# Kernel tuning notes

Measured on AMD Instinct MI355X. Metric: run time of the kernel, lower is better.

## Reference

```python
import jax, jax.numpy as jnp
from jax import lax
import numpy as np

B, D, P = 4096, 256, 512  # batch, encoded_space_dim (=d_prototypes), n_prototypes
BN_EPS = 1e-5  # torch BatchNorm eval with running_mean=0, running_var=1


def _conv(x, w, stride, pad):
    # x: NCHW, w: OIHW
    return lax.conv_general_dilated(x, w, (stride, stride), [(pad, pad), (pad, pad)],
                                    dimension_numbers=('NCHW', 'OIHW', 'NCHW'))


def _conv_t(x, w, stride, pad, out_pad):
    # torch ConvTranspose2d; w in torch layout [Cin, Cout, kh, kw]
    k = w.shape[2]
    wf = jnp.flip(w, (2, 3)).transpose(1, 0, 2, 3)  # -> OIHW, flipped
    lo = k - 1 - pad
    hi = k - 1 - pad + out_pad
    return lax.conv_general_dilated(x, wf, (1, 1), [(lo, hi), (lo, hi)],
                                    lhs_dilation=(stride, stride),
                                    dimension_numbers=('NCHW', 'OIHW', 'NCHW'))


def _bn(x, g, b):
    # eval-mode BatchNorm2d with running_mean=0, running_var=1
    s = g / jnp.sqrt(1.0 + BN_EPS)
    return x * s[None, :, None, None] + b[None, :, None, None]


def _bias(x, b):
    return x + b[None, :, None, None]


def setup_inputs() -> dict:
    key = jax.random.key(0)
    ks = jax.random.split(key, 32)
    n = jax.random.normal
    inp = {
        'x': jax.random.uniform(ks[0], (B, 1, 28, 28), jnp.float32),
        # encoder
        'w1': n(ks[1], (8, 1, 3, 3), jnp.float32) * 0.1, 'b1': jnp.zeros((8,), jnp.float32),
        'w2': n(ks[2], (16, 8, 3, 3), jnp.float32) * 0.1, 'b2': jnp.zeros((16,), jnp.float32),
        'g2': jnp.ones((16,), jnp.float32), 'bt2': jnp.zeros((16,), jnp.float32),
        'w3': n(ks[3], (D, 16, 3, 3), jnp.float32) * 0.1, 'b3': jnp.zeros((D,), jnp.float32),
        # prototypes (torch.rand init)
        'protolayer': jax.random.uniform(ks[4], (P, D, 1, 1), jnp.float32),
        # up layer (ConvTranspose2d(D, D, 5), torch layout [Cin,Cout,kh,kw])
        'wup': n(ks[5], (D, D, 5, 5), jnp.float32) * 0.02, 'bup': jnp.zeros((D,), jnp.float32),
        'gup': jnp.ones((D,), jnp.float32), 'btup': jnp.zeros((D,), jnp.float32),
        # decoder
        'wd1': n(ks[6], (D, 16, 3, 3), jnp.float32) * 0.05, 'bd1': jnp.zeros((16,), jnp.float32),
        'gd1': jnp.ones((16,), jnp.float32), 'btd1': jnp.zeros((16,), jnp.float32),
        'wd2': n(ks[7], (16, 8, 3, 3), jnp.float32) * 0.1, 'bd2': jnp.zeros((8,), jnp.float32),
        'gd2': jnp.ones((8,), jnp.float32), 'btd2': jnp.zeros((8,), jnp.float32),
        'wd3': n(ks[8], (8, 1, 3, 3), jnp.float32) * 0.1, 'bd3': jnp.zeros((1,), jnp.float32),
    }
    return inp


def reference(x, w1, b1, w2, b2, g2, bt2, w3, b3, protolayer,
              wup, bup, gup, btup,
              wd1, bd1, gd1, btd1, wd2, bd2, gd2, btd2, wd3, bd3):
    # ---- encoder: 28 -> 14 -> 7 -> 5 ----
    h = jax.nn.relu(_bias(_conv(x, w1, 2, 1), b1))
    h = jax.nn.relu(_bn(_bias(_conv(h, w2, 2, 1), b2), g2, bt2))
    h = jax.nn.relu(_bias(_conv(h, w3, 1, 0), b3))  # [B, D, 5, 5]

    # ---- l2 'convolution' with 1x1 prototypes ----
    p = protolayer[:, :, 0, 0]                                  # [P, D]
    x2_patch_sum = jnp.sum(h * h, axis=1)                       # ones-conv, 1x1 kernel -> channel sum [B,5,5]
    xp = jnp.einsum('bdhw,pd->bphw', h, p)                      # [B, P, 5, 5]
    p2 = jnp.sum(p * p, axis=1)                                 # [P]
    distances = jax.nn.relu(x2_patch_sum[:, None] - 2.0 * xp + p2[None, :, None, None])

    # min-pool over full spatial extent
    min_distances = jnp.min(distances, axis=(2, 3))             # [B, P]
    prototype_activations = -min_distances                      # 'linear' distance_2_similarity
    w = jax.nn.softmax(prototype_activations, axis=1)
    z = jnp.einsum('bp,pdkl->bdkl', w, protolayer)              # [B, D, 1, 1]

    # ---- up layer: 1 -> 5 ----
    z = jax.nn.relu(_bn(_bias(_conv_t(z, wup, 1, 0, 0), bup), gup, btup))

    # ---- decoder: 5 -> 7 -> 14 -> 28 ----
    h = jax.nn.relu(_bn(_bias(_conv_t(z, wd1, 1, 0, 0), bd1), gd1, btd1))
    h = jax.nn.relu(_bn(_bias(_conv_t(h, wd2, 2, 1, 1), bd2), gd2, btd2))
    out = jax.nn.sigmoid(_bias(_conv_t(h, wd3, 2, 1, 1), bd3))  # [B, 1, 28, 28]
    return out, min_distances
```

## Files before the change

kernel.cpp:

```cpp
#include <hip/hip_runtime.h>
#include <hip/hip_bf16.h>
#include <math.h>

#define NB 4096
#define DC 256
#define PC 512

typedef unsigned short ushort_t;
typedef __attribute__((ext_vector_type(4))) unsigned short us4;
typedef __attribute__((ext_vector_type(8))) unsigned short us8;
typedef __attribute__((ext_vector_type(8))) short s8v;
typedef __attribute__((ext_vector_type(4))) float f32x4;

__device__ __forceinline__ float bf16_to_f(ushort_t u) {
    union { unsigned int i; float f; } c;
    c.i = ((unsigned int)u) << 16;
    return c.f;
}
__device__ __forceinline__ ushort_t f2bf(float f) {
    union { float f; unsigned int u; } c; c.f = f;
    unsigned int r = c.u + 0x7fffu + ((c.u >> 16) & 1u);
    return (ushort_t)(r >> 16);
}

__global__ __launch_bounds__(256) void k_pre(
    const float* __restrict__ proto, float* __restrict__ p2,
    ushort_t* __restrict__ pfragHi, ushort_t* __restrict__ pfragLo,
    const float* __restrict__ w3, ushort_t* __restrict__ w3fH, ushort_t* __restrict__ w3fL,
    const float* __restrict__ w2, ushort_t* __restrict__ w2fH, ushort_t* __restrict__ w2fL,
    const float* __restrict__ wd1, ushort_t* __restrict__ wd1frag,
    const float* __restrict__ wup, ushort_t* __restrict__ wupfH, ushort_t* __restrict__ wupfL)
{
    int b = blockIdx.x, tid = threadIdx.x;
    __shared__ float red[256];
    if (b < 512) {
        int p = b, d = tid;
        float v = proto[p * DC + d];
        red[d] = v * v;
        __syncthreads();
        for (int s = 128; s > 0; s >>= 1) {
            if (d < s) red[d] += red[d + s];
            __syncthreads();
        }
        if (d == 0) p2[p] = red[0];
    } else if (b < 1024) {
        int idx = (b - 512) * 256 + tid;
        int j = idx & 7, l = (idx >> 3) & 63;
        int k0 = (idx >> 9) & 7, nt = idx >> 12;
        int n = nt * 16 + (l & 15);
        int k = k0 * 32 + (l >> 4) * 8 + j;
        float v = proto[n * DC + k];
        ushort_t hi = f2bf(v);
        pfragHi[idx] = hi;
        pfragLo[idx] = f2bf(v - bf16_to_f(hi));
    } else if (b < 1184) {
        int idx = (b - 1024) * 256 + tid;
        int j = idx & 7, l = (idx >> 3) & 63;
        int q = idx >> 9;
        int k0 = q % 5, nt = q / 5;
        int d = nt * 16 + (l & 15);
        int k = k0 * 32 + (l >> 4) * 8 + j;
        float v = (k < 144) ? w3[d * 144 + k] : 0.f;
        ushort_t hi = f2bf(v);
        w3fH[idx] = hi;
        w3fL[idx] = f2bf(v - bf16_to_f(hi));
    } else if (b < 1190) {
        int idx = (b - 1184) * 256 + tid;
        int j = idx & 7, l = (idx >> 3) & 63;
        int k0 = idx >> 9;
        int ch = l & 15;
        int k = k0 * 32 + (l >> 4) * 8 + j;
        float v = (k < 72) ? w2[ch * 72 + k] : 0.f;
        ushort_t hi = f2bf(v);
        w2fH[idx] = hi;
        w2fL[idx] = f2bf(v - bf16_to_f(hi));
    } else if (b < 1334) {
        int idx = (b - 1190) * 256 + tid;
        int j = idx & 7, l = (idx >> 3) & 63;
        int k0 = (idx >> 9) & 7, nt = idx >> 12;
        int n = nt * 16 + (l & 15);
        int k = k0 * 32 + (l >> 4) * 8 + j;
        wd1frag[idx] = f2bf(wd1[k * 144 + n]);
    } else {
        int idx = (b - 1334) * 256 + tid;
        int j = idx & 7, l = (idx >> 3) & 63;
        int k0 = (idx >> 9) & 7, nt = idx >> 12;
        int np = nt * 16 + (l & 15);
        int d = k0 * 32 + (l >> 4) * 8 + j;
        int pos = np >> 8, ch = np & 255;
        float v = wup[d * 6400 + ch * 25 + pos];
        ushort_t hi = f2bf(v);
        wupfH[idx] = hi;
        wupfL[idx] = f2bf(v - bf16_to_f(hi));
    }
}

__global__ __launch_bounds__(256) void k_pw2(
    const ushort_t* __restrict__ pfragHi, const ushort_t* __restrict__ pfragLo,
    const ushort_t* __restrict__ wupfH, const ushort_t* __restrict__ wupfL,
    ushort_t* __restrict__ PWfrag)
{
    int t = threadIdx.x;
    int w = t >> 6, l = t & 63, lr = l & 15, lg = l >> 4;
    int my = blockIdx.y;
    int ntb = blockIdx.x * 16 + w * 4;
    const s8v* AH = (const s8v*)pfragHi;
    const s8v* AL = (const s8v*)pfragLo;
    const s8v* BH = (const s8v*)wupfH;
    const s8v* BL = (const s8v*)wupfL;
    f32x4 acc[4];
#pragma unroll
    for (int q = 0; q < 4; q++) acc[q] = (f32x4){0.f, 0.f, 0.f, 0.f};
#pragma unroll
    for (int k0 = 0; k0 < 8; k0++) {
        s8v ah = AH[(my * 8 + k0) * 64 + l];
        s8v al = AL[(my * 8 + k0) * 64 + l];
#pragma unroll
        for (int q = 0; q < 4; q++) {
            s8v bh = BH[(size_t)((ntb + q) * 8 + k0) * 64 + l];
            s8v bl = BL[(size_t)((ntb + q) * 8 + k0) * 64 + l];
            acc[q] = __builtin_amdgcn_mfma_f32_16x16x32_bf16(ah, bh, acc[q], 0, 0, 0);
            acc[q] = __builtin_amdgcn_mfma_f32_16x16x32_bf16(al, bh, acc[q], 0, 0, 0);
            acc[q] = __builtin_amdgcn_mfma_f32_16x16x32_bf16(ah, bl, acc[q], 0, 0, 0);
        }
    }
#pragma unroll
    for (int q = 0; q < 4; q++) {
        int nt = ntb + q;
#pragma unroll
        for (int r = 0; r < 4; r++) {
            int p = my * 16 + lg * 4 + r;
            int k0p = p >> 5;
            int ll = ((p >> 3) & 3) * 16 + lr;
            int jj = p & 7;
            PWfrag[(((size_t)(nt * 16 + k0p) * 64) + ll) * 8 + jj] = f2bf(acc[q][r]);
        }
    }
}

__global__ __launch_bounds__(512) void k_enc1(
    const float* __restrict__ x,
    const float* __restrict__ w1, const float* __restrict__ b1,
    const ushort_t* __restrict__ w2fH, const ushort_t* __restrict__ w2fL,
    const float* __restrict__ b2,
    const float* __restrict__ g2, const float* __restrict__ bt2,
    const ushort_t* __restrict__ w3fH, const ushort_t* __restrict__ w3fL,
    const float* __restrict__ b3,
    ushort_t* __restrict__ h3g)
{
    int b0 = blockIdx.x * 2;
    int t = threadIdx.x;
    int w = t >> 6, l = t & 63, lr = l & 15, lg = l >> 4;
    int tim = t >> 8, tt = t & 255;

    __shared__ __align__(16) unsigned char buf[51712];
    unsigned char* bufI = buf + tim * 25856;
    float* xb = (float*)bufI;
    float* h1 = (float*)(bufI + 3136);
    ushort_t* im2Hi = (ushort_t*)(bufI + 9408);
    float* h2 = (float*)(bufI + 22720);
    ushort_t* imHi = (ushort_t*)bufI;

    const float bnr = rsqrtf(1.0f + 1e-5f);

    const float* xg = x + (size_t)(b0 + tim) * 784;
    for (int i = tt; i < 784; i += 256) xb[i] = xg[i];
    for (int i = tt; i < 832; i += 256)
        ((float4*)(bufI + 9408))[i] = (float4){0.f, 0.f, 0.f, 0.f};
    __syncthreads();

    for (int o = tt; o < 1568; o += 256) {
        int c = o / 196, r = o % 196, y = r / 14, xc = r % 14;
        float acc = b1[c];
        for (int sy = 0; sy < 3; sy++) {
            int iy = 2 * y - 1 + sy;
            if ((unsigned)iy >= 28u) continue;
            for (int sx = 0; sx < 3; sx++) {
                int ix = 2 * xc - 1 + sx;
                if ((unsigned)ix >= 28u) continue;
                acc += w1[c * 9 + sy * 3 + sx] * xb[iy * 28 + ix];
            }
        }
        float v = fmaxf(acc, 0.f);
        ushort_t hi = f2bf(v);
        int kb = c * 9;
        int yA, syA, xA, sxA, yB = 0, xB = 0;
        bool hasYB, hasXB;
        if (y & 1) { yA = y >> 1; syA = 2; yB = yA + 1; hasYB = (yB < 7); }
        else       { yA = y >> 1; syA = 1; hasYB = false; }
        if (xc & 1) { xA = xc >> 1; sxA = 2; xB = xA + 1; hasXB = (xB < 7); }
        else        { xA = xc >> 1; sxA = 1; hasXB = false; }
        im2Hi[(yA * 7 + xA) * 104 + kb + syA * 3 + sxA] = hi;
        if (hasXB) im2Hi[(yA * 7 + xB) * 104 + kb + syA * 3] = hi;
        if (hasYB) {
            im2Hi[(yB * 7 + xA) * 104 + kb + sxA] = hi;
            if (hasXB) im2Hi[(yB * 7 + xB) * 104 + kb] = hi;
        }
    }
    __syncthreads();

    {
        int w4 = w & 3;
        f32x4 cc = {0, 0, 0, 0};
        const s8v* WH = (const s8v*)w2fH;
        const s8v* WL = (const s8v*)w2fL;
#pragma unroll
        for (int k0 = 0; k0 < 3; k0++) {
            s8v a0 = *(const s8v*)&im2Hi[(w4 * 16 + lr) * 104 + k0 * 32 + lg * 8];
            s8v bh = WH[k0 * 64 + l];
            s8v bl = WL[k0 * 64 + l];
            cc = __builtin_amdgcn_mfma_f32_16x16x32_bf16(a0, bh, cc, 0, 0, 0);
            cc = __builtin_amdgcn_mfma_f32_16x16x32_bf16(a0, bl, cc, 0, 0, 0);
        }
        int ch = lr;
        float s = g2[ch] * bnr, bb = b2[ch], bt = bt2[ch];
#pragma unroll
        for (int r = 0; r < 4; r++) {
            int pos = w4 * 16 + lg * 4 + r;
            if (pos < 49)
                h2[ch * 49 + pos] = fmaxf((cc[r] + bb) * s + bt, 0.f);
        }
    }
    __syncthreads();

    if (tt < 16) imHi[3600 + tt] = 0;
    for (int o = tt; o < 784; o += 256) {
        float v = h2[o];
        int ci = o / 49, rr = o % 49, iy = rr / 7, ixp = rr % 7;
        ushort_t hi = f2bf(v);
        int kb = ci * 9;
#pragma unroll
        for (int sy = 0; sy < 3; sy++) {
            int py = iy - sy;
            if ((unsigned)py < 5u) {
#pragma unroll
                for (int sx = 0; sx < 3; sx++) {
                    int px = ixp - sx;
                    if ((unsigned)px < 5u)
                        imHi[(py * 5 + px) * 144 + kb + sy * 3 + sx] = hi;
                }
            }
        }
    }
    __syncthreads();

    {
        const ushort_t* imHi0 = (const ushort_t*)buf;
        const ushort_t* imHi1 = (const ushort_t*)(buf + 25856);
        int nt0 = 2 * w;
        f32x4 c[2][2][2];
#pragma unroll
        for (int im = 0; im < 2; im++)
#pragma unroll
            for (int q = 0; q < 2; q++)
#pragma unroll
                for (int mt = 0; mt < 2; mt++) c[im][q][mt] = (f32x4){0.f, 0.f, 0.f, 0.f};
        const s8v* WH = (const s8v*)w3fH;
        const s8v* WL = (const s8v*)w3fL;
#pragma unroll
        for (int k0 = 0; k0 < 5; k0++) {
            s8v a00 = *(const s8v*)&imHi0[lr * 144 + k0 * 32 + lg * 8];
            s8v a01 = *(const s8v*)&imHi0[(16 + lr) * 144 + k0 * 32 + lg * 8];
            s8v a10 = *(const s8v*)&imHi1[lr * 144 + k0 * 32 + lg * 8];
            s8v a11 = *(const s8v*)&imHi1[(16 + lr) * 144 + k0 * 32 + lg * 8];
            s8v bh0 = WH[(nt0 * 5 + k0) * 64 + l];
            s8v bl0 = WL[(nt0 * 5 + k0) * 64 + l];
            s8v bh1 = WH[((nt0 + 1) * 5 + k0) * 64 + l];
            s8v bl1 = WL[((nt0 + 1) * 5 + k0) * 64 + l];
            c[0][0][0] = __builtin_amdgcn_mfma_f32_16x16x32_bf16(a00, bh0, c[0][0][0], 0, 0, 0);
            c[0][0][1] = __builtin_amdgcn_mfma_f32_16x16x32_bf16(a01, bh0, c[0][0][1], 0, 0, 0);
            c[0][0][0] = __builtin_amdgcn_mfma_f32_16x16x32_bf16(a00, bl0, c[0][0][0], 0, 0, 0);
            c[0][0][1] = __builtin_amdgcn_mfma_f32_16x16x32_bf16(a01, bl0, c[0][0][1], 0, 0, 0);
            c[0][1][0] = __builtin_amdgcn_mfma_f32_16x16x32_bf16(a00, bh1, c[0][1][0], 0, 0, 0);
            c[0][1][1] = __builtin_amdgcn_mfma_f32_16x16x32_bf16(a01, bh1, c[0][1][1], 0, 0, 0);
            c[0][1][0] = __builtin_amdgcn_mfma_f32_16x16x32_bf16(a00, bl1, c[0][1][0], 0, 0, 0);
            c[0][1][1] = __builtin_amdgcn_mfma_f32_16x16x32_bf16(a01, bl1, c[0][1][1], 0, 0, 0);
            c[1][0][0] = __builtin_amdgcn_mfma_f32_16x16x32_bf16(a10, bh0, c[1][0][0], 0, 0, 0);
            c[1][0][1] = __builtin_amdgcn_mfma_f32_16x16x32_bf16(a11, bh0, c[1][0][1], 0, 0, 0);
            c[1][0][0] = __builtin_amdgcn_mfma_f32_16x16x32_bf16(a10, bl0, c[1][0][0], 0, 0, 0);
            c[1][0][1] = __builtin_amdgcn_mfma_f32_16x16x32_bf16(a11, bl0, c[1][0][1], 0, 0, 0);
            c[1][1][0] = __builtin_amdgcn_mfma_f32_16x16x32_bf16(a10, bh1, c[1][1][0], 0, 0, 0);
            c[1][1][1] = __builtin_amdgcn_mfma_f32_16x16x32_bf16(a11, bh1, c[1][1][1], 0, 0, 0);
            c[1][1][0] = __builtin_amdgcn_mfma_f32_16x16x32_bf16(a10, bl1, c[1][1][0], 0, 0, 0);
            c[1][1][1] = __builtin_amdgcn_mfma_f32_16x16x32_bf16(a11, bl1, c[1][1][1], 0, 0, 0);
        }
#pragma unroll
        for (int im = 0; im < 2; im++) {
            ushort_t* hg = h3g + (size_t)(b0 + im) * 6400;
#pragma unroll
            for (int q = 0; q < 2; q++) {
                int d = (nt0 + q) * 16 + lr;
                float bb = b3[d];
#pragma unroll
                for (int mt = 0; mt < 2; mt++) {
                    f32x4 cv = c[im][q][mt];
#pragma unroll
                    for (int r = 0; r < 4; r++) {
                        int pos = mt * 16 + lg * 4 + r;
                        if (pos < 25) {
                            float h = fmaxf(cv[r] + bb, 0.f);
                            hg[pos * 256 + d] = f2bf(h);
                        }
                    }
                }
            }
        }
    }
}

__global__ __launch_bounds__(1024) void k_enc2(
    const ushort_t* __restrict__ h3g,
    const ushort_t* __restrict__ pfragHi,
    const float* __restrict__ p2,
    float* __restrict__ md_out,
    ushort_t* __restrict__ Wsm)
{
    int t = threadIdx.x;
    int b0 = blockIdx.x * 2;
    int w = t >> 6, l = t & 63, lr = l & 15, lg = l >> 4;

    __shared__ __align__(16) ushort_t h3s[2][32][264];
    __shared__ float mds[2][512];
    __shared__ float x2sh[2][32];
    __shared__ float x2part[2][25][8];
    __shared__ float wred[2][16];

    for (int i = t; i < 2048; i += 1024) {
        int im = i >> 10, pos = (i >> 5) & 31, c8 = i & 31;
        us8 v = {0, 0, 0, 0, 0, 0, 0, 0};
        if (pos < 25)
            v = *(const us8*)&h3g[(size_t)(b0 + im) * 6400 + pos * 256 + c8 * 8];
        *(us8*)&h3s[im][pos][c8 * 8] = v;
    }
    __syncthreads();

    if (t < 400) {
        int im = t / 200, rest = t % 200;
        int pos = rest >> 3, ch = rest & 7;
        const ushort_t* hp = &h3s[im][pos][ch * 32];
        float s = 0.f;
#pragma unroll
        for (int i = 0; i < 32; i++) {
            float f = bf16_to_f(hp[i]);
            s = fmaf(f, f, s);
        }
        x2part[im][pos][ch] = s;
    }
    __syncthreads();
    if (t < 64) {
        int im = t >> 5, pos = t & 31;
        float s = 1e30f;
        if (pos < 25) {
            s = 0.f;
#pragma unroll
            for (int c = 0; c < 8; c++) s += x2part[im][pos][c];
        }
        x2sh[im][pos] = s;
    }
    __syncthreads();

    {
        f32x4 acc[2][2][2];
#pragma unroll
        for (int i = 0; i < 2; i++)
#pragma unroll
            for (int jm = 0; jm < 2; jm++)
#pragma unroll
                for (int mt = 0; mt < 2; mt++) acc[i][jm][mt] = (f32x4){0.f, 0.f, 0.f, 0.f};
        const s8v* BH = (const s8v*)pfragHi;
        s8v bhc[2], bhn[2];
#pragma unroll
        for (int ntq = 0; ntq < 2; ntq++) {
            int nt = w * 2 + ntq;
            bhc[ntq] = BH[(nt * 8 + 0) * 64 + l];
        }
        for (int k0 = 0; k0 < 8; k0++) {
            if (k0 < 7) {
#pragma unroll
                for (int ntq = 0; ntq < 2; ntq++) {
                    int nt = w * 2 + ntq;
                    bhn[ntq] = BH[(nt * 8 + k0 + 1) * 64 + l];
                }
            }
            s8v ah[2][2];
            ah[0][0] = *(const s8v*)&h3s[0][lr][k0 * 32 + lg * 8];
            ah[0][1] = *(const s8v*)&h3s[0][16 + lr][k0 * 32 + lg * 8];
            ah[1][0] = *(const s8v*)&h3s[1][lr][k0 * 32 + lg * 8];
            ah[1][1] = *(const s8v*)&h3s[1][16 + lr][k0 * 32 + lg * 8];
#pragma unroll
            for (int ntq = 0; ntq < 2; ntq++) {
                s8v bh = bhc[ntq];
#pragma unroll
                for (int im = 0; im < 2; im++) {
                    acc[ntq][im][0] = __builtin_amdgcn_mfma_f32_16x16x32_bf16(ah[im][0], bh, acc[ntq][im][0], 0, 0, 0);
                    acc[ntq][im][1] = __builtin_amdgcn_mfma_f32_16x16x32_bf16(ah[im][1], bh, acc[ntq][im][1], 0, 0, 0);
                }
            }
#pragma unroll
            for (int ntq = 0; ntq < 2; ntq++) bhc[ntq] = bhn[ntq];
        }
        float x2r[2][8];
#pragma unroll
        for (int im = 0; im < 2; im++)
#pragma unroll
            for (int r = 0; r < 4; r++) {
                x2r[im][r]     = x2sh[im][lg * 4 + r];
                x2r[im][4 + r] = x2sh[im][16 + lg * 4 + r];
            }
#pragma unroll
        for (int ntq = 0; ntq < 2; ntq++) {
            int pcol = (w * 2 + ntq) * 16 + lr;
            float p2v = p2[pcol];
#pragma unroll
            for (int im = 0; im < 2; im++) {
                float mm = 1e30f;
#pragma unroll
                for (int r = 0; r < 4; r++) {
                    float d0 = fmaxf(x2r[im][r]     - 2.f * acc[ntq][im][0][r] + p2v, 0.f);
                    float d1 = fmaxf(x2r[im][4 + r] - 2.f * acc[ntq][im][1][r] + p2v, 0.f);
                    mm = fminf(mm, fminf(d0, d1));
                }
                mm = fminf(mm, __shfl_xor(mm, 16));
                mm = fminf(mm, __shfl_xor(mm, 32));
                if (lg == 0) mds[im][pcol] = mm;
            }
        }
    }
    __syncthreads();

    int img = t >> 9, tt = t & 511;
    float mind = mds[img][tt];
    md_out[(size_t)(b0 + img) * PC + tt] = mind;
    float a = -mind;
    float mx = a;
#pragma unroll
    for (int off = 1; off < 64; off <<= 1) mx = fmaxf(mx, __shfl_xor(mx, off));
    int wv = w & 7;
    if (l == 0) wred[img][wv] = mx;
    __syncthreads();
    float m = wred[img][0];
#pragma unroll
    for (int i = 1; i < 8; i++) m = fmaxf(m, wred[img][i]);
    float e = expf(a - m);
    float sm = e;
#pragma unroll
    for (int off = 1; off < 64; off <<= 1) sm += __shfl_xor(sm, off);
    if (l == 0) wred[img][8 + wv] = sm;
    __syncthreads();
    float ssum = wred[img][8];
#pragma unroll
    for (int i = 9; i < 16; i++) ssum += wred[img][i];
    Wsm[(size_t)(b0 + img) * PC + tt] = f2bf(e / ssum);
}

__global__ __launch_bounds__(512) void k_zup2(
    const ushort_t* __restrict__ Wsm,
    const ushort_t* __restrict__ PWfrag,
    const float* __restrict__ bup, const float* __restrict__ gup,
    const float* __restrict__ btup,
    ushort_t* __restrict__ zupT)
{
    __shared__ __align__(16) ushort_t Bsh[2][8192];
    int t = threadIdx.x;
    int w = t >> 6, l = t & 63;
    int n0 = blockIdx.x * 128;
    int m0 = blockIdx.y * 128;
    int row = m0 + w * 16 + (l & 15);
    int krow = (l >> 4) * 8;
    f32x4 acc[8];
#pragma unroll
    for (int i = 0; i < 8; i++) acc[i] = (f32x4){0.f, 0.f, 0.f, 0.f};
    const s8v* B = (const s8v*)PWfrag;
    int base = blockIdx.x * 8 * 16;

    {
        s8v v0 = B[(size_t)(base + (t >> 6) * 16 + 0) * 64 + (t & 63)];
        s8v v1 = B[(size_t)(base + (t >> 6) * 16 + 1) * 64 + (t & 63)];
        *(s8v*)&Bsh[0][t * 8] = v0;
        *(s8v*)&Bsh[0][4096 + t * 8] = v1;
    }
    __syncthreads();
    for (int r = 0; r < 8; r++) {
        int cur = r & 1;
        if (r < 7) {
            s8v v0 = B[(size_t)(base + (t >> 6) * 16 + 2 * r + 2) * 64 + (t & 63)];
            s8v v1 = B[(size_t)(base + (t >> 6) * 16 + 2 * r + 3) * 64 + (t & 63)];
            *(s8v*)&Bsh[cur ^ 1][t * 8] = v0;
            *(s8v*)&Bsh[cur ^ 1][4096 + t * 8] = v1;
        }
#pragma unroll
        for (int kk = 0; kk < 2; kk++) {
            int k0 = 2 * r + kk;
            s8v a = *(const s8v*)&Wsm[(size_t)row * 512 + k0 * 32 + krow];
#pragma unroll
            for (int nt = 0; nt < 8; nt++) {
                s8v bb = *(const s8v*)&Bsh[cur][kk * 4096 + (nt * 64 + l) * 8];
                acc[nt] = __builtin_amdgcn_mfma_f32_16x16x32_bf16(a, bb, acc[nt], 0, 0, 0);
            }
        }
        __syncthreads();
    }

    const float bnr = rsqrtf(1.0f + 1e-5f);
    int rowbase = m0 + w * 16 + (l >> 4) * 4;
#pragma unroll
    for (int nt = 0; nt < 8; nt++) {
        int n = n0 + nt * 16 + (l & 15);
        int ch = n & 255;
        float sc = gup[ch] * bnr, bb = bup[ch], bt = btup[ch];
#pragma unroll
        for (int r = 0; r < 4; r++) {
            float v = (acc[nt][r] + bb) * sc + bt;
            zupT[(size_t)(rowbase + r) * 6400 + n] = f2bf(fmaxf(v, 0.f));
        }
    }
}

template<int CLS, int NCO>
__device__ __forceinline__ void wd2_piece(
    const float* hb, float* hout, const float* w2sT,
    const float* bd2, const float* gd2, const float* btd2,
    float bnr, int r, int c, int co0)
{
    const int cy = CLS >> 1, cx = CLS & 1;
    float acc[NCO];
#pragma unroll
    for (int q = 0; q < NCO; q++) acc[q] = 0.f;
#pragma unroll
    for (int ty = 0; ty < 1 + cy; ty++) {
        int iy = r + ty;
        int sy = cy ? (ty ? 0 : 2) : 1;
#pragma unroll
        for (int tx = 0; tx < 1 + cx; tx++) {
            int ix = c + tx;
            int sx = cx ? (tx ? 0 : 2) : 1;
            const float* wp = &w2sT[(sy * 3 + sx) * 128];
            int hoff = iy * 8 + ix;
            float h[16];
#pragma unroll
            for (int ci = 0; ci < 16; ci++) h[ci] = hb[ci * 64 + hoff];
#pragma unroll
            for (int q = 0; q < NCO; q++) {
                const float* wc = &wp[(co0 + q) * 16];
                float a = acc[q];
#pragma unroll
                for (int ci = 0; ci < 16; ci++) a = fmaf(h[ci], wc[ci], a);
                acc[q] = a;
            }
        }
    }
    int y = 2 * r + cy, x = 2 * c + cx;
#pragma unroll
    for (int q = 0; q < NCO; q++) {
        int co = co0 + q;
        float v = (acc[q] + bd2[co]) * (gd2[co] * bnr) + btd2[co];
        hout[co * 225 + y * 15 + x] = fmaxf(v, 0.f);
    }
}

template<int CLS, int NROW>
__device__ __forceinline__ void wd3_piece(
    const float* h2b, const float* w3sT, float bd30,
    float* og, int l, int row0)
{
    const int cy = CLS >> 1, cx = CLS & 1;
    const int NIT = (NROW * 16 + 63) / 64;
#pragma unroll
    for (int j = 0; j < NIT; j++) {
        int idx = l + 64 * j;
        int row = idx >> 4, col = idx & 15;
        if (row < NROW && col < 14) {
            int rr = row0 + row;
            float a = bd30;
#pragma unroll
            for (int ty = 0; ty < 1 + cy; ty++) {
                int iy = rr + ty;
                int sy = cy ? (ty ? 0 : 2) : 1;
#pragma unroll
                for (int tx = 0; tx < 1 + cx; tx++) {
                    int ix = col + tx;
                    int sx = cx ? (tx ? 0 : 2) : 1;
                    const float* wp = &w3sT[(sy * 3 + sx) * 8];
                    int hoff = iy * 15 + ix;
#pragma unroll
                    for (int ci = 0; ci < 8; ci++)
                        a = fmaf(h2b[ci * 225 + hoff], wp[ci], a);
                }
            }
            int y = 2 * rr + cy, x = 2 * col + cx;
            og[y * 28 + x] = 1.f / (1.f + expf(-a));
        }
    }
}

__global__ __launch_bounds__(512) void k_dtail(
    const ushort_t* __restrict__ zupT,
    const ushort_t* __restrict__ wd1frag,
    const float* __restrict__ bd1, const float* __restrict__ gd1, const float* __restrict__ btd1,
    const float* __restrict__ wd2, const float* __restrict__ bd2,
    const float* __restrict__ gd2, const float* __restrict__ btd2,
    const float* __restrict__ wd3, const float* __restrict__ bd3,
    float* __restrict__ out0)
{
    int b0 = blockIdx.x * 2, t = threadIdx.x;
    int w = t >> 6, l = t & 63, lr = l & 15, lg = l >> 4;
    int g = w >> 2, wv = w & 3, tg = t & 255;
    __shared__ __align__(16) unsigned char dbuf[33792];
    __shared__ float hd1p[2][16][64];
    __shared__ float w2sT[9 * 8 * 16];
    __shared__ float w3sT[9 * 8];
    ushort_t* zAb = (ushort_t*)dbuf;
    float* Psb = (float*)dbuf;

    const float bnr = rsqrtf(1.0f + 1e-5f);

    for (int c = t; c < 1600; c += 512) {
        int im = c / 800, cc = c % 800;
        *(us8*)&zAb[im * 8448 + (cc >> 5) * 264 + (cc & 31) * 8] =
            *(const us8*)&zupT[(size_t)(b0 + im) * 6400 + cc * 8];
    }
    for (int i = t; i < 2048; i += 512) ((float*)hd1p)[i] = 0.f;
    for (int i = t; i < 1152; i += 512) {
        int s = i >> 7, rest = i & 127;
        int co = rest >> 4, ci = rest & 15;
        w2sT[i] = wd2[(ci * 8 + co) * 9 + s];
    }
    if (t < 72) {
        int s = t >> 3, ci = t & 7;
        w3sT[t] = wd3[ci * 9 + s];
    }
    __syncthreads();

    {
        f32x4 acc[3][2];
#pragma unroll
        for (int i = 0; i < 3; i++)
#pragma unroll
            for (int mt = 0; mt < 2; mt++) acc[i][mt] = (f32x4){0.f, 0.f, 0.f, 0.f};
        const s8v* B = (const s8v*)wd1frag;
        for (int k0 = 0; k0 < 8; k0++) {
            s8v a0 = *(const s8v*)&zAb[g * 8448 + lr * 264 + k0 * 32 + lg * 8];
            s8v a1 = *(const s8v*)&zAb[g * 8448 + (16 + lr) * 264 + k0 * 32 + lg * 8];
#pragma unroll
            for (int i = 0; i < 3; i++) {
                int nt = wv + 4 * i;
                if (nt < 9) {
                    s8v bb = B[(nt * 8 + k0) * 64 + l];
                    acc[i][0] = __builtin_amdgcn_mfma_f32_16x16x32_bf16(a0, bb, acc[i][0], 0, 0, 0);
                    acc[i][1] = __builtin_amdgcn_mfma_f32_16x16x32_bf16(a1, bb, acc[i][1], 0, 0, 0);
                }
            }
        }
        __syncthreads();
#pragma unroll
        for (int i = 0; i < 3; i++) {
            int nt = wv + 4 * i;
            if (nt < 9) {
                int col = nt * 16 + lr;
#pragma unroll
                for (int mt = 0; mt < 2; mt++)
#pragma unroll
                    for (int r = 0; r < 4; r++) {
                        int pos = mt * 16 + lg * 4 + r;
                        if (pos < 25) Psb[g * 3700 + pos * 148 + col] = acc[i][mt][r];
                    }
            }
        }
    }
    __syncthreads();

    for (int o = tg; o < 784; o += 256) {
        int co = o / 49, rr = o % 49, y = rr / 7, xx = rr % 7;
        float a = bd1[co];
        int sy0 = y - 4 > 0 ? y - 4 : 0, sy1 = y < 2 ? y : 2;
        for (int sy = sy0; sy <= sy1; sy++) {
            int iy = y - sy;
            int sx0 = xx - 4 > 0 ? xx - 4 : 0, sx1 = xx < 2 ? xx : 2;
            for (int sx = sx0; sx <= sx1; sx++) {
                int ix = xx - sx;
                a += Psb[g * 3700 + (iy * 5 + ix) * 148 + co * 9 + sy * 3 + sx];
            }
        }
        float v = a * (gd1[co] * bnr) + btd1[co];
        hd1p[g][co][y * 8 + xx] = fmaxf(v, 0.f);
    }
    __syncthreads();

    {
        if (t < 464) {
            int im = t / 232, rest = t % 232;
            int co = rest / 29, s = rest % 29;
            int yy = (s < 15) ? 14 : (s - 15);
            int xx2 = (s < 15) ? s : 14;
            ((float*)dbuf)[im * 1808 + co * 225 + yy * 15 + xx2] = 0.f;
        }
        if (l < 56 && (l & 7) < 7) {
            int r = l >> 3, c = l & 7;
            const float* hb = &hd1p[g][0][0];
            float* hout = (float*)dbuf + g * 1808;
            if (wv == 0) {
                wd2_piece<3, 4>(hb, hout, w2sT, bd2, gd2, btd2, bnr, r, c, 0);
                wd2_piece<0, 2>(hb, hout, w2sT, bd2, gd2, btd2, bnr, r, c, 0);
            } else if (wv == 1) {
                wd2_piece<3, 4>(hb, hout, w2sT, bd2, gd2, btd2, bnr, r, c, 4);
                wd2_piece<0, 2>(hb, hout, w2sT, bd2, gd2, btd2, bnr, r, c, 2);
            } else if (wv == 2) {
                wd2_piece<1, 8>(hb, hout, w2sT, bd2, gd2, btd2, bnr, r, c, 0);
                wd2_piece<0, 2>(hb, hout, w2sT, bd2, gd2, btd2, bnr, r, c, 4);
            } else {
                wd2_piece<2, 8>(hb, hout, w2sT, bd2, gd2, btd2, bnr, r, c, 0);
                wd2_piece<0, 2>(hb, hout, w2sT, bd2, gd2, btd2, bnr, r, c, 6);
            }
        }
    }
    __syncthreads();

    {
        const float* h2b = (const float*)dbuf + g * 1808;
        float* og = out0 + (size_t)(b0 + g) * 784;
        float bd30 = bd3[0];
        if (wv == 0) {
            wd3_piece<3, 7>(h2b, w3sT, bd30, og, l, 0);
            wd3_piece<0, 7>(h2b, w3sT, bd30, og, l, 0);
        } else if (wv == 1) {
            wd3_piece<3, 7>(h2b, w3sT, bd30, og, l, 7);
            wd3_piece<0, 7>(h2b, w3sT, bd30, og, l, 7);
        } else if (wv == 2) {
            wd3_piece<1, 14>(h2b, w3sT, bd30, og, l, 0);
        } else {
            wd3_piece<2, 14>(h2b, w3sT, bd30, og, l, 0);
        }
    }
}

extern "C" void kernel_launch(void* const* d_in, const int* in_sizes, int n_in,
                              void* d_out, int out_size, void* d_ws, size_t ws_size,
                              hipStream_t stream) {
    const float* x    = (const float*)d_in[0];
    const float* w1   = (const float*)d_in[1];
    const float* b1   = (const float*)d_in[2];
    const float* w2   = (const float*)d_in[3];
    const float* b2   = (const float*)d_in[4];
    const float* g2   = (const float*)d_in[5];
    const float* bt2  = (const float*)d_in[6];
    const float* w3   = (const float*)d_in[7];
    const float* b3   = (const float*)d_in[8];
    const float* proto= (const float*)d_in[9];
    const float* wup  = (const float*)d_in[10];
    const float* bup  = (const float*)d_in[11];
    const float* gup  = (const float*)d_in[12];
    const float* btup = (const float*)d_in[13];
    const float* wd1  = (const float*)d_in[14];
    const float* bd1  = (const float*)d_in[15];
    const float* gd1  = (const float*)d_in[16];
    const float* btd1 = (const float*)d_in[17];
    const float* wd2  = (const float*)d_in[18];
    const float* bd2  = (const float*)d_in[19];
    const float* gd2  = (const float*)d_in[20];
    const float* btd2 = (const float*)d_in[21];
    const float* wd3  = (const float*)d_in[22];
    const float* bd3  = (const float*)d_in[23];

    float* out0   = (float*)d_out;
    float* out_md = out0 + (size_t)NB * 784;

    float*    p2      = (float*)d_ws;
    float*    pad0    = p2 + 512;
    ushort_t* pfragHi = (ushort_t*)(pad0 + 131072);
    ushort_t* pfragLo = pfragHi + 131072;
    ushort_t* w3fH    = pfragLo + 131072;
    ushort_t* w3fL    = w3fH + 40960;
    ushort_t* w2fH    = w3fL + 40960;
    ushort_t* w2fL    = w2fH + 1536;
    ushort_t* wd1frag = w2fL + 1536;
    ushort_t* wupfH   = wd1frag + 36864;
    ushort_t* wupfL   = wupfH + 1638400;
    ushort_t* PWfrag  = wupfL + 1638400;
    ushort_t* Wsm     = PWfrag + 3276800;
    ushort_t* BIG     = Wsm + 2097152;
    ushort_t* h3g     = BIG;
    ushort_t* zupT    = BIG;

    hipLaunchKernelGGL(k_pre, dim3(7734), dim3(256), 0, stream,
                       proto, p2, pfragHi, pfragLo, w3, w3fH, w3fL,
                       w2, w2fH, w2fL, wd1, wd1frag, wup, wupfH, wupfL);
    hipLaunchKernelGGL(k_pw2, dim3(25, 32), dim3(256), 0, stream,
                       pfragHi, pfragLo, wupfH, wupfL, PWfrag);
    hipLaunchKernelGGL(k_enc1, dim3(NB / 2), dim3(512), 0, stream,
                       x, w1, b1, w2fH, w2fL, b2, g2, bt2, w3fH, w3fL, b3, h3g);
    hipLaunchKernelGGL(k_enc2, dim3(NB / 2), dim3(1024), 0, stream,
                       h3g, pfragHi, p2, out_md, Wsm);
    hipLaunchKernelGGL(k_zup2, dim3(50, 32), dim3(512), 0, stream,
                       Wsm, PWfrag, bup, gup, btup, zupT);
    hipLaunchKernelGGL(k_dtail, dim3(NB / 2), dim3(512), 0, stream,
                       zupT, wd1frag, bd1, gd1, btd1, wd2, bd2, gd2, btd2, wd3, bd3, out0);
}
```

Measured before the change: 242.6 us.

## Double k_enc1 block to 1024 threads and stage h3 output through LDS

```diff
diff --git a/kernel.cpp b/kernel.cpp
--- a/kernel.cpp
+++ b/kernel.cpp
@@ -138,7 +138,7 @@
     }
 }
 
-__global__ __launch_bounds__(512) void k_enc1(
+__global__ __launch_bounds__(1024) void k_enc1(
     const float* __restrict__ x,
     const float* __restrict__ w1, const float* __restrict__ b1,
     const ushort_t* __restrict__ w2fH, const ushort_t* __restrict__ w2fL,
@@ -151,7 +151,7 @@
     int b0 = blockIdx.x * 2;
     int t = threadIdx.x;
     int w = t >> 6, l = t & 63, lr = l & 15, lg = l >> 4;
-    int tim = t >> 8, tt = t & 255;
+    int tim = t >> 9, tt = t & 511;
 
     __shared__ __align__(16) unsigned char buf[51712];
     unsigned char* bufI = buf + tim * 25856;
@@ -164,12 +164,12 @@
     const float bnr = rsqrtf(1.0f + 1e-5f);
 
     const float* xg = x + (size_t)(b0 + tim) * 784;
-    for (int i = tt; i < 784; i += 256) xb[i] = xg[i];
-    for (int i = tt; i < 832; i += 256)
+    for (int i = tt; i < 784; i += 512) xb[i] = xg[i];
+    for (int i = tt; i < 832; i += 512)
         ((float4*)(bufI + 9408))[i] = (float4){0.f, 0.f, 0.f, 0.f};
     __syncthreads();
 
-    for (int o = tt; o < 1568; o += 256) {
+    for (int o = tt; o < 1568; o += 512) {
         int c = o / 196, r = o % 196, y = r / 14, xc = r % 14;
         float acc = b1[c];
         for (int sy = 0; sy < 3; sy++) {
@@ -199,7 +199,7 @@
     }
     __syncthreads();
 
-    {
+    if ((w & 7) < 4) {
         int w4 = w & 3;
         f32x4 cc = {0, 0, 0, 0};
         const s8v* WH = (const s8v*)w2fH;
@@ -223,8 +223,8 @@
     }
     __syncthreads();
 
-    if (tt < 16) imHi[3600 + tt] = 0;
-    for (int o = tt; o < 784; o += 256) {
+    if (tt < 64) imHi[3600 + tt] = 0;
+    for (int o = tt; o < 784; o += 512) {
         float v = h2[o];
         int ci = o / 49, rr = o % 49, iy = rr / 7, ixp = rr % 7;
         ushort_t hi = f2bf(v);
@@ -247,14 +247,12 @@
     {
         const ushort_t* imHi0 = (const ushort_t*)buf;
         const ushort_t* imHi1 = (const ushort_t*)(buf + 25856);
-        int nt0 = 2 * w;
-        f32x4 c[2][2][2];
+        int nt = w;
+        f32x4 c[2][2];
 #pragma unroll
         for (int im = 0; im < 2; im++)
 #pragma unroll
-            for (int q = 0; q < 2; q++)
-#pragma unroll
-                for (int mt = 0; mt < 2; mt++) c[im][q][mt] = (f32x4){0.f, 0.f, 0.f, 0.f};
+            for (int mt = 0; mt < 2; mt++) c[im][mt] = (f32x4){0.f, 0.f, 0.f, 0.f};
         const s8v* WH = (const s8v*)w3fH;
         const s8v* WL = (const s8v*)w3fL;
 #pragma unroll
@@ -263,48 +261,44 @@
             s8v a01 = *(const s8v*)&imHi0[(16 + lr) * 144 + k0 * 32 + lg * 8];
             s8v a10 = *(const s8v*)&imHi1[lr * 144 + k0 * 32 + lg * 8];
             s8v a11 = *(const s8v*)&imHi1[(16 + lr) * 144 + k0 * 32 + lg * 8];
-            s8v bh0 = WH[(nt0 * 5 + k0) * 64 + l];
-            s8v bl0 = WL[(nt0 * 5 + k0) * 64 + l];
-            s8v bh1 = WH[((nt0 + 1) * 5 + k0) * 64 + l];
-            s8v bl1 = WL[((nt0 + 1) * 5 + k0) * 64 + l];
-            c[0][0][0] = __builtin_amdgcn_mfma_f32_16x16x32_bf16(a00, bh0, c[0][0][0], 0, 0, 0);
-            c[0][0][1] = __builtin_amdgcn_mfma_f32_16x16x32_bf16(a01, bh0, c[0][0][1], 0, 0, 0);
-            c[0][0][0] = __builtin_amdgcn_mfma_f32_16x16x32_bf16(a00, bl0, c[0][0][0], 0, 0, 0);
-            c[0][0][1] = __builtin_amdgcn_mfma_f32_16x16x32_bf16(a01, bl0, c[0][0][1], 0, 0, 0);
-            c[0][1][0] = __builtin_amdgcn_mfma_f32_16x16x32_bf16(a00, bh1, c[0][1][0], 0, 0, 0);
-            c[0][1][1] = __builtin_amdgcn_mfma_f32_16x16x32_bf16(a01, bh1, c[0][1][1], 0, 0, 0);
-            c[0][1][0] = __builtin_amdgcn_mfma_f32_16x16x32_bf16(a00, bl1, c[0][1][0], 0, 0, 0);
-            c[0][1][1] = __builtin_amdgcn_mfma_f32_16x16x32_bf16(a01, bl1, c[0][1][1], 0, 0, 0);
-            c[1][0][0] = __builtin_amdgcn_mfma_f32_16x16x32_bf16(a10, bh0, c[1][0][0], 0, 0, 0);
-            c[1][0][1] = __builtin_amdgcn_mfma_f32_16x16x32_bf16(a11, bh0, c[1][0][1], 0, 0, 0);
-            c[1][0][0] = __builtin_amdgcn_mfma_f32_16x16x32_bf16(a10, bl0, c[1][0][0], 0, 0, 0);
-            c[1][0][1] = __builtin_amdgcn_mfma_f32_16x16x32_bf16(a11, bl0, c[1][0][1], 0, 0, 0);
-            c[1][1][0] = __builtin_amdgcn_mfma_f32_16x16x32_bf16(a10, bh1, c[1][1][0], 0, 0, 0);
-            c[1][1][1] = __builtin_amdgcn_mfma_f32_16x16x32_bf16(a11, bh1, c[1][1][1], 0, 0, 0);
-            c[1][1][0] = __builtin_amdgcn_mfma_f32_16x16x32_bf16(a10, bl1, c[1][1][0], 0, 0, 0);
-            c[1][1][1] = __builtin_amdgcn_mfma_f32_16x16x32_bf16(a11, bl1, c[1][1][1], 0, 0, 0);
-        }
+            s8v bh = WH[(nt * 5 + k0) * 64 + l];
+            s8v bl = WL[(nt * 5 + k0) * 64 + l];
+            c[0][0] = __builtin_amdgcn_mfma_f32_16x16x32_bf16(a00, bh, c[0][0], 0, 0, 0);
+            c[0][1] = __builtin_amdgcn_mfma_f32_16x16x32_bf16(a01, bh, c[0][1], 0, 0, 0);
+            c[0][0] = __builtin_amdgcn_mfma_f32_16x16x32_bf16(a00, bl, c[0][0], 0, 0, 0);
+            c[0][1] = __builtin_amdgcn_mfma_f32_16x16x32_bf16(a01, bl, c[0][1], 0, 0, 0);
+            c[1][0] = __builtin_amdgcn_mfma_f32_16x16x32_bf16(a10, bh, c[1][0], 0, 0, 0);
+            c[1][1] = __builtin_amdgcn_mfma_f32_16x16x32_bf16(a11, bh, c[1][1], 0, 0, 0);
+            c[1][0] = __builtin_amdgcn_mfma_f32_16x16x32_bf16(a10, bl, c[1][0], 0, 0, 0);
+            c[1][1] = __builtin_amdgcn_mfma_f32_16x16x32_bf16(a11, bl, c[1][1], 0, 0, 0);
+        }
+        __syncthreads();
+        int d = nt * 16 + lr;
+        float bb = b3[d];
 #pragma unroll
         for (int im = 0; im < 2; im++) {
-            ushort_t* hg = h3g + (size_t)(b0 + im) * 6400;
-#pragma unroll
-            for (int q = 0; q < 2; q++) {
-                int d = (nt0 + q) * 16 + lr;
-                float bb = b3[d];
-#pragma unroll
-                for (int mt = 0; mt < 2; mt++) {
-                    f32x4 cv = c[im][q][mt];
-#pragma unroll
-                    for (int r = 0; r < 4; r++) {
-                        int pos = mt * 16 + lg * 4 + r;
-                        if (pos < 25) {
-                            float h = fmaxf(cv[r] + bb, 0.f);
-                            hg[pos * 256 + d] = f2bf(h);
-                        }
+            ushort_t* hs = (ushort_t*)(buf + im * 25856);
+#pragma unroll
+            for (int mt = 0; mt < 2; mt++) {
+                f32x4 cv = c[im][mt];
+#pragma unroll
+                for (int r = 0; r < 4; r++) {
+                    int pos = mt * 16 + lg * 4 + r;
+                    if (pos < 25) {
+                        float h = fmaxf(cv[r] + bb, 0.f);
+                        hs[pos * 256 + d] = f2bf(h);
                     }
                 }
             }
         }
+    }
+    __syncthreads();
+
+    for (int i = t; i < 1600; i += 1024) {
+        int im = i >= 800 ? 1 : 0;
+        int idx = im ? i - 800 : i;
+        *(us8*)&h3g[(size_t)(b0 + im) * 6400 + idx * 8] =
+            *(const us8*)((const ushort_t*)(buf + im * 25856) + idx * 8);
     }
 }
 
@@ -786,7 +780,7 @@
                        w2, w2fH, w2fL, wd1, wd1frag, wup, wupfH, wupfL);
     hipLaunchKernelGGL(k_pw2, dim3(25, 32), dim3(256), 0, stream,
                        pfragHi, pfragLo, wupfH, wupfL, PWfrag);
-    hipLaunchKernelGGL(k_enc1, dim3(NB / 2), dim3(512), 0, stream,
+    hipLaunchKernelGGL(k_enc1, dim3(NB / 2), dim3(1024), 0, stream,
                        x, w1, b1, w2fH, w2fL, b2, g2, bt2, w3fH, w3fL, b3, h3g);
     hipLaunchKernelGGL(k_enc2, dim3(NB / 2), dim3(1024), 0, stream,
                        h3g, pfragHi, p2, out_md, Wsm);
```

Result: faster. 237.3 us, median of 2 (-2.2%).
